# Performance work log

Measured on AMD Instinct MI355X. Metric: run time of the kernel, lower is better.

The kernel has to match this reference:

```python
import jax, jax.numpy as jnp
import numpy as np

N_EXPERTS = 8
D_MODEL = 1024
D_FF = 4096
TOP_K = 2
B, S = 1, 2048


def setup_inputs() -> dict:
    key = jax.random.key(0)
    ks = jax.random.split(key, 5)
    scale_in = 1.0 / np.sqrt(D_MODEL)
    scale_ff = 1.0 / np.sqrt(D_FF)
    return {
        "x": jax.random.normal(ks[0], (B, S, D_MODEL), dtype=jnp.float32),
        "w_gate": jax.random.normal(ks[1], (D_MODEL, N_EXPERTS), dtype=jnp.float32) * scale_in,
        "b_gate": jnp.zeros((N_EXPERTS,), dtype=jnp.float32),
        "w1": jax.random.normal(ks[2], (N_EXPERTS, D_MODEL, D_FF), dtype=jnp.float32) * scale_in,
        "b1": jnp.zeros((N_EXPERTS, D_FF), dtype=jnp.float32),
        "w2": jax.random.normal(ks[3], (N_EXPERTS, D_FF, D_MODEL), dtype=jnp.float32) * scale_ff,
        "b2": jnp.zeros((N_EXPERTS, D_MODEL), dtype=jnp.float32),
    }


def reference(x, w_gate, b_gate, w1, b1, w2, b2):
    d = x.shape[-1]
    xs = x.reshape(-1, d)                       # [T, d]
    T = xs.shape[0]

    # --- routing: top-k gate logits, softmax over the k selected slots ---
    gate_logits = xs @ w_gate + b_gate          # [T, E]
    topk_vals, topk_idx = jax.lax.top_k(gate_logits, TOP_K)   # [T, k]
    weights = jax.nn.softmax(topk_vals, axis=-1)              # [T, k]

    # scatter slot weights into a dense [T, E] combine matrix
    comb = jnp.zeros((T, N_EXPERTS), dtype=xs.dtype)
    comb = comb.at[jnp.arange(T)[:, None], topk_idx].add(weights)

    # --- expert FFNs computed densely, combined with routing weights ---
    h = jax.nn.relu(jnp.einsum('td,edf->etf', xs, w1) + b1[:, None, :])  # [E, T, ff]
    y = jnp.einsum('etf,efd->etd', h, w2) + b2[:, None, :]               # [E, T, d]
    out = jnp.einsum('te,etd->td', comb, y)                              # [T, d]
    return out.reshape(x.shape)
```

## Files before the change

### kernel.cpp

```cpp
#include <hip/hip_runtime.h>
#include <hip/hip_bf16.h>
#include <math.h>

#define T_TOK 2048
#define DM    1024
#define DF    4096
#define NE    8
#define BM    128
#define BN    128
#define BK    64
#define LDA2  72
#define LDAV1 40

typedef __attribute__((ext_vector_type(8))) short          bf16x8;
typedef __attribute__((ext_vector_type(8))) unsigned short ushort8;
typedef __attribute__((ext_vector_type(4))) float          f32x4;

__device__ __forceinline__ unsigned short f2bf(float f) {
  unsigned u = __builtin_bit_cast(unsigned, f);
  unsigned r = u + 0x7fffu + ((u >> 16) & 1u);
  return (unsigned short)(r >> 16);
}

__global__ void convert_x_kernel(const float* __restrict__ x, unsigned short* __restrict__ xb) {
  int i = blockIdx.x * blockDim.x + threadIdx.x;
  const float* src = x + (size_t)i * 8;
  float4 a = *(const float4*)(src);
  float4 b = *(const float4*)(src + 4);
  ushort8 v;
  v[0] = f2bf(a.x); v[1] = f2bf(a.y); v[2] = f2bf(a.z); v[3] = f2bf(a.w);
  v[4] = f2bf(b.x); v[5] = f2bf(b.y); v[6] = f2bf(b.z); v[7] = f2bf(b.w);
  *(ushort8*)(xb + (size_t)i * 8) = v;
}

template<int K, int N>
__global__ __launch_bounds__(256) void transpose_convert_packed(
    const float* __restrict__ W, unsigned short* __restrict__ Wt)
{
  const int e  = blockIdx.z;
  const int kt = blockIdx.y;
  const int nt = blockIdx.x;
  const int k0 = kt * 64;
  const int n0 = nt * 128;
  const float* Wp = W + (size_t)e * K * N;
  __shared__ float Ls[64][129];
  const int tid = threadIdx.x;
  {
    const int kl = tid >> 5;
    const int nl = (tid & 31) * 4;
#pragma unroll
    for (int p = 0; p < 8; p++) {
      const int k = kl + p * 8;
      float4 v = *(const float4*)(Wp + (size_t)(k0 + k) * N + n0 + nl);
      Ls[k][nl + 0] = v.x; Ls[k][nl + 1] = v.y; Ls[k][nl + 2] = v.z; Ls[k][nl + 3] = v.w;
    }
  }
  __syncthreads();
  unsigned short* Wo = Wt + ((((size_t)e * (N / 128) + nt) * (K / 64) + kt) * 128) * 64;
  {
    const int n  = tid & 127;
    const int c0 = tid >> 7;
#pragma unroll
    for (int p = 0; p < 4; p++) {
      const int c = c0 + p * 2;
      ushort8 o;
#pragma unroll
      for (int j = 0; j < 8; j++) o[j] = f2bf(Ls[c * 8 + j][n]);
      *(ushort8*)(Wo + (size_t)n * 64 + c * 8) = o;
    }
  }
}

__global__ __launch_bounds__(256) void gating_kernel(
    const float* __restrict__ x, const float* __restrict__ wg, const float* __restrict__ bg,
    int* __restrict__ cnt, int* __restrict__ perm, float* __restrict__ pw)
{
  int wid  = (blockIdx.x * blockDim.x + threadIdx.x) >> 6;
  int lane = threadIdx.x & 63;
  if (wid >= T_TOK) return;
  const float* xr = x + (size_t)wid * DM;

  float acc[NE];
#pragma unroll
  for (int e = 0; e < NE; e++) acc[e] = 0.f;

  for (int d = lane; d < DM; d += 64) {
    float xv = xr[d];
    const float* wr = wg + (size_t)d * NE;
#pragma unroll
    for (int e = 0; e < NE; e++) acc[e] += xv * wr[e];
  }
#pragma unroll
  for (int off = 32; off > 0; off >>= 1) {
#pragma unroll
    for (int e = 0; e < NE; e++) acc[e] += __shfl_xor(acc[e], off, 64);
  }
  if (lane == 0) {
    float v[NE];
#pragma unroll
    for (int e = 0; e < NE; e++) v[e] = acc[e] + bg[e];
    int i0 = 0; float v0 = v[0];
#pragma unroll
    for (int e = 1; e < NE; e++) { if (v[e] > v0) { v0 = v[e]; i0 = e; } }
    int i1 = -1; float v1 = -INFINITY;
#pragma unroll
    for (int e = 0; e < NE; e++) { if (e != i0 && v[e] > v1) { v1 = v[e]; i1 = e; } }
    float e1 = expf(v1 - v0);
    float s  = 1.f + e1;
    float w0 = 1.f / s, w1 = e1 / s;
    int p0 = atomicAdd(&cnt[i0], 1);
    perm[i0 * T_TOK + p0] = wid; pw[i0 * T_TOK + p0] = w0;
    int p1 = atomicAdd(&cnt[i1], 1);
    perm[i1 * T_TOK + p1] = wid; pw[i1 * T_TOK + p1] = w1;
  }
}

__global__ void pad_scan_kernel(const int* __restrict__ cnt, int* __restrict__ cntpad,
                                int* __restrict__ offs, int* __restrict__ perm, float* __restrict__ pw)
{
  if (threadIdx.x == 0) {
    int o = 0;
    for (int e = 0; e < NE; e++) {
      int c  = cnt[e];
      int cp = (c + BM - 1) / BM * BM;
      cntpad[e] = cp;
      offs[e]   = o;
      o += cp;
    }
    offs[NE] = o;
  }
  for (int e = 0; e < NE; e++) {
    int c  = cnt[e];
    int cp = (c + BM - 1) / BM * BM;
    for (int i = c + threadIdx.x; i < cp; i += blockDim.x) {
      perm[e * T_TOK + i] = 0;
      pw[e * T_TOK + i]   = 0.f;
    }
  }
}

template<int PHASE, int KTOT, int NCOLS, int KSPLIT>
__global__ __launch_bounds__(256, 3) void moe_gemm4(
    const unsigned short* __restrict__ Asrc,
    const unsigned short* __restrict__ Bt,
    const float* __restrict__ bias,
    const int* __restrict__ cntpad, const int* __restrict__ offs,
    const int* __restrict__ perm, const float* __restrict__ pw,
    unsigned short* __restrict__ Hout, float* __restrict__ out)
{
  const int e  = blockIdx.z;
  const int mt = blockIdx.y;
  const int nt = blockIdx.x / KSPLIT;
  const int ks = blockIdx.x % KSPLIT;
  const int cp = cntpad[e];
  if (mt * BM >= cp) return;
  const int tid = threadIdx.x;
  const int oe  = offs[e];

  __shared__ unsigned short As[BM * LDA2];
  __shared__ unsigned short Bs[BN * LDA2];

  const int am = tid >> 1;
  const int ak = (tid & 1) * 32;
  const int kb0 = ks * (KTOT / KSPLIT);
  const int KITERS = (KTOT / KSPLIT) / BK;

  const unsigned short* Ap;
  size_t APITCH;
  if (PHASE == 1) {
    int token = perm[e * T_TOK + mt * BM + am];
    Ap = Asrc + (size_t)token * KTOT + kb0 + ak;
    APITCH = BK;
  } else {
    const size_t rb = (size_t)(oe >> 7) + mt;
    Ap = Asrc + (((rb * (KTOT / 64) + (kb0 >> 6)) * 128 + am) * 64) + ak;
    APITCH = (size_t)128 * 64;
  }
  const unsigned short* Bp =
      Bt + ((((size_t)e * (NCOLS / 128) + nt) * (KTOT / 64) + (kb0 >> 6)) * 128 + am) * 64 + ak;

  const int wid  = tid >> 6;
  const int lane = tid & 63;
  const int wm   = (wid & 1) * 64;
  const int wn   = (wid >> 1) * 64;
  const int lrow = lane & 15;
  const int lk   = (lane >> 4) * 8;

  f32x4 acc[4][4];
#pragma unroll
  for (int i = 0; i < 4; i++)
#pragma unroll
    for (int j = 0; j < 4; j++) acc[i][j] = (f32x4){0.f, 0.f, 0.f, 0.f};

  uint4 pa0, pa1, pa2, pa3, pb0, pb1, pb2, pb3;
  auto LOADT = [&](int kt) {
    const unsigned short* a = Ap + (size_t)kt * APITCH;
    const unsigned short* b = Bp + (size_t)kt * (128 * 64);
    pa0 = *(const uint4*)(a);      pa1 = *(const uint4*)(a + 8);
    pa2 = *(const uint4*)(a + 16); pa3 = *(const uint4*)(a + 24);
    pb0 = *(const uint4*)(b);      pb1 = *(const uint4*)(b + 8);
    pb2 = *(const uint4*)(b + 16); pb3 = *(const uint4*)(b + 24);
  };
  auto STORET = [&]() {
    unsigned short* as = &As[am * LDA2 + ak];
    unsigned short* bs = &Bs[am * LDA2 + ak];
    *(uint4*)(as)      = pa0; *(uint4*)(as + 8)  = pa1;
    *(uint4*)(as + 16) = pa2; *(uint4*)(as + 24) = pa3;
    *(uint4*)(bs)      = pb0; *(uint4*)(bs + 8)  = pb1;
    *(uint4*)(bs + 16) = pb2; *(uint4*)(bs + 24) = pb3;
  };

  LOADT(0);
  STORET();
  for (int kt = 0; kt < KITERS; kt++) {
    __syncthreads();
    if (kt + 1 < KITERS) LOADT(kt + 1);
#pragma unroll
    for (int ksb = 0; ksb < 2; ksb++) {
      bf16x8 af[4], bfr[4];
#pragma unroll
      for (int i = 0; i < 4; i++)
        af[i]  = *(const bf16x8*)&As[(wm + i * 16 + lrow) * LDA2 + ksb * 32 + lk];
#pragma unroll
      for (int j = 0; j < 4; j++)
        bfr[j] = *(const bf16x8*)&Bs[(wn + j * 16 + lrow) * LDA2 + ksb * 32 + lk];
#pragma unroll
      for (int i = 0; i < 4; i++)
#pragma unroll
        for (int j = 0; j < 4; j++)
          acc[i][j] = __builtin_amdgcn_mfma_f32_16x16x32_bf16(af[i], bfr[j], acc[i][j], 0, 0, 0);
    }
    __syncthreads();
    if (kt + 1 < KITERS) STORET();
  }

  const int crow = (lane >> 4) * 4;
  const int ccol = lane & 15;
  const size_t rbh = (size_t)(oe >> 7) + mt;
#pragma unroll
  for (int j = 0; j < 4; j++) {
    const int gn = nt * BN + wn + j * 16 + ccol;
    const float bv = bias[e * NCOLS + gn];
#pragma unroll
    for (int i = 0; i < 4; i++) {
#pragma unroll
      for (int r = 0; r < 4; r++) {
        const int lm = wm + i * 16 + crow + r;
        float v = acc[i][j][r];
        if (PHASE == 1) {
          v += bv;
          v = v > 0.f ? v : 0.f;
          Hout[(((rbh * (NCOLS / 64) + (gn >> 6)) * 128 + lm) * 64) + (gn & 63)] = f2bf(v);
        } else {
          if (ks == 0) v += bv;
          const int li    = e * T_TOK + mt * BM + lm;
          const int token = perm[li];
          const float w   = pw[li];
          atomicAdd(&out[(size_t)token * NCOLS + gn], w * v);
        }
      }
    }
  }
}

template<int PHASE, int KTOT, int NCOLS, int KSPLIT>
__global__ __launch_bounds__(256) void moe_gemm_v1(
    const unsigned short* __restrict__ Asrc,
    const float* __restrict__ Wbase,
    const float* __restrict__ bias,
    const int* __restrict__ cntpad, const int* __restrict__ offs,
    const int* __restrict__ perm, const float* __restrict__ pw,
    unsigned short* __restrict__ Hout, float* __restrict__ out)
{
  const int e  = blockIdx.z;
  const int mt = blockIdx.y;
  const int nt = blockIdx.x / KSPLIT;
  const int ks = blockIdx.x % KSPLIT;
  const int cp = cntpad[e];
  if (mt * BM >= cp) return;
  const int tid = threadIdx.x;
  const int oe  = offs[e];

  __shared__ unsigned short As[BM * LDAV1];
  __shared__ unsigned short Bs[BN * LDAV1];

  const int am = tid >> 1;
  const int ak = (tid & 1) * 16;
  size_t arow_off;
  if (PHASE == 1) {
    int token = perm[e * T_TOK + mt * BM + am];
    arow_off = (size_t)token * KTOT;
  } else {
    arow_off = (size_t)(oe + mt * BM + am) * (size_t)KTOT;
  }
  const int bn  = tid & 127;
  const int bk0 = (tid >> 7) * 16;
  const float* Wexp = Wbase + (size_t)e * KTOT * NCOLS + (size_t)nt * BN;
  const int kbase0 = ks * (KTOT / KSPLIT);
  const int KITERS = (KTOT / KSPLIT) / 32;
  const int wid  = tid >> 6;
  const int lane = tid & 63;
  const int wm   = (wid & 1) * 64;
  const int wn   = (wid >> 1) * 64;
  const int lrow = lane & 15;
  const int lk   = (lane >> 4) * 8;

  f32x4 acc[4][4];
#pragma unroll
  for (int i = 0; i < 4; i++)
#pragma unroll
    for (int j = 0; j < 4; j++) acc[i][j] = (f32x4){0.f, 0.f, 0.f, 0.f};

  for (int kt = 0; kt < KITERS; kt++) {
    const int kb = kbase0 + kt * 32;
    {
      const unsigned short* src = Asrc + arow_off + kb + ak;
      uint4 v0 = *(const uint4*)(src);
      uint4 v1 = *(const uint4*)(src + 8);
      *(uint4*)&As[am * LDAV1 + ak]     = v0;
      *(uint4*)&As[am * LDAV1 + ak + 8] = v1;
    }
#pragma unroll
    for (int t2 = 0; t2 < 2; t2++) {
      const int kk = bk0 + t2 * 8;
      const float* wp = Wexp + (size_t)(kb + kk) * NCOLS + bn;
      ushort8 tv;
#pragma unroll
      for (int j = 0; j < 8; j++) tv[j] = f2bf(wp[(size_t)j * NCOLS]);
      *(ushort8*)&Bs[bn * LDAV1 + kk] = tv;
    }
    __syncthreads();
    bf16x8 af[4], bfr[4];
#pragma unroll
    for (int i = 0; i < 4; i++) af[i]  = *(const bf16x8*)&As[(wm + i * 16 + lrow) * LDAV1 + lk];
#pragma unroll
    for (int j = 0; j < 4; j++) bfr[j] = *(const bf16x8*)&Bs[(wn + j * 16 + lrow) * LDAV1 + lk];
#pragma unroll
    for (int i = 0; i < 4; i++)
#pragma unroll
      for (int j = 0; j < 4; j++)
        acc[i][j] = __builtin_amdgcn_mfma_f32_16x16x32_bf16(af[i], bfr[j], acc[i][j], 0, 0, 0);
    __syncthreads();
  }

  const int crow = (lane >> 4) * 4;
  const int ccol = lane & 15;
#pragma unroll
  for (int j = 0; j < 4; j++) {
    const int gn = nt * BN + wn + j * 16 + ccol;
    const float bv = bias[e * NCOLS + gn];
#pragma unroll
    for (int i = 0; i < 4; i++) {
#pragma unroll
      for (int r = 0; r < 4; r++) {
        const int lm = wm + i * 16 + crow + r;
        float v = acc[i][j][r];
        if (PHASE == 1) {
          v += bv;
          v = v > 0.f ? v : 0.f;
          Hout[(size_t)(oe + mt * BM + lm) * NCOLS + gn] = f2bf(v);
        } else {
          if (ks == 0) v += bv;
          const int li    = e * T_TOK + mt * BM + lm;
          const int token = perm[li];
          const float w   = pw[li];
          atomicAdd(&out[(size_t)token * NCOLS + gn], w * v);
        }
      }
    }
  }
}

extern "C" void kernel_launch(void* const* d_in, const int* in_sizes, int n_in,
                              void* d_out, int out_size, void* d_ws, size_t ws_size,
                              hipStream_t stream) {
  const float* x  = (const float*)d_in[0];
  const float* wg = (const float*)d_in[1];
  const float* bg = (const float*)d_in[2];
  const float* w1 = (const float*)d_in[3];
  const float* b1 = (const float*)d_in[4];
  const float* w2 = (const float*)d_in[5];
  const float* b2 = (const float*)d_in[6];
  float* out = (float*)d_out;

  const size_t XB_BYTES   = (size_t)T_TOK * DM * 2;
  const size_t PERM_BYTES = (size_t)NE * T_TOK * 4;
  const size_t PW_BYTES   = (size_t)NE * T_TOK * 4;
  const size_t H_BYTES    = (size_t)(2 * T_TOK + NE * BM) * DF * 2;
  const size_t W1T_BYTES  = (size_t)NE * DF * DM * 2;
  const size_t W2T_BYTES  = (size_t)NE * DM * DF * 2;

  char* wsp = (char*)d_ws;
  size_t off = 0;
  unsigned short* xb = (unsigned short*)(wsp + off); off += XB_BYTES;
  int*   cnt    = (int*)(wsp + off); off += 256;
  int*   cntpad = cnt + 8;
  int*   offs   = cnt + 16;
  int*   perm   = (int*)(wsp + off);   off += PERM_BYTES;
  float* pwt    = (float*)(wsp + off); off += PW_BYTES;
  unsigned short* H   = (unsigned short*)(wsp + off); off += H_BYTES;
  unsigned short* w1t = (unsigned short*)(wsp + off); off += W1T_BYTES;
  unsigned short* w2t = (unsigned short*)(wsp + off); off += W2T_BYTES;
  const size_t REQUIRED = off;

  hipMemsetAsync(cnt, 0, 256, stream);
  hipMemsetAsync(d_out, 0, (size_t)T_TOK * DM * 4, stream);

  convert_x_kernel<<<(T_TOK * DM / 8) / 256, 256, 0, stream>>>(x, xb);
  gating_kernel<<<T_TOK / 4, 256, 0, stream>>>(x, wg, bg, cnt, perm, pwt);
  pad_scan_kernel<<<1, 256, 0, stream>>>(cnt, cntpad, offs, perm, pwt);

  if (ws_size >= REQUIRED) {
    transpose_convert_packed<DM, DF><<<dim3(DF / 128, DM / 64, NE), 256, 0, stream>>>(w1, w1t);
    transpose_convert_packed<DF, DM><<<dim3(DM / 128, DF / 64, NE), 256, 0, stream>>>(w2, w2t);

    moe_gemm4<1, DM, DF, 1><<<dim3(DF / BN, T_TOK / BM, NE), 256, 0, stream>>>(
        xb, w1t, b1, cntpad, offs, perm, pwt, H, nullptr);
    moe_gemm4<2, DF, DM, 2><<<dim3((DM / BN) * 2, T_TOK / BM, NE), 256, 0, stream>>>(
        H, w2t, b2, cntpad, offs, perm, pwt, nullptr, out);
  } else {
    moe_gemm_v1<1, DM, DF, 1><<<dim3(DF / BN, T_TOK / BM, NE), 256, 0, stream>>>(
        xb, w1, b1, cntpad, offs, perm, pwt, H, nullptr);
    moe_gemm_v1<2, DF, DM, 4><<<dim3((DM / BN) * 4, T_TOK / BM, NE), 256, 0, stream>>>(
        H, w2, b2, cntpad, offs, perm, pwt, nullptr, out);
  }
}
```

Baseline: 629.4 us.

## Replace atomic scatter in second GEMM with split-K buffers and gather combine

The second expert GEMM now writes its per-slot outputs into two dense fp32 buffers, one per K-split, that reuse the w1t workspace, instead of atomically adding weighted results into the output. Gating records each token's slot indices and weights, and a new combine kernel gathers the two expert rows per token, sums the split halves and applies the routing weights. This removes contended fp32 atomics in the GEMM epilogue. In exchange it adds an extra kernel launch and a full write and read of the intermediate buffers. It also relies on w1t being dead after the first GEMM, and the output memset is now redundant.

```diff
diff --git a/kernel.cpp b/kernel.cpp
--- a/kernel.cpp
+++ b/kernel.cpp
@@ -11,6 +11,7 @@
 #define BK    64
 #define LDA2  72
 #define LDAV1 40
+#define YROWS 5120
 
 typedef __attribute__((ext_vector_type(8))) short          bf16x8;
 typedef __attribute__((ext_vector_type(8))) unsigned short ushort8;
@@ -73,7 +74,8 @@
 
 __global__ __launch_bounds__(256) void gating_kernel(
     const float* __restrict__ x, const float* __restrict__ wg, const float* __restrict__ bg,
-    int* __restrict__ cnt, int* __restrict__ perm, float* __restrict__ pw)
+    int* __restrict__ cnt, int* __restrict__ perm, float* __restrict__ pw,
+    int* __restrict__ tok2slot, float* __restrict__ tokw)
 {
   int wid  = (blockIdx.x * blockDim.x + threadIdx.x) >> 6;
   int lane = threadIdx.x & 63;
@@ -112,6 +114,8 @@
     perm[i0 * T_TOK + p0] = wid; pw[i0 * T_TOK + p0] = w0;
     int p1 = atomicAdd(&cnt[i1], 1);
     perm[i1 * T_TOK + p1] = wid; pw[i1 * T_TOK + p1] = w1;
+    tok2slot[2 * wid + 0] = (i0 << 16) | p0;  tokw[2 * wid + 0] = w0;
+    tok2slot[2 * wid + 1] = (i1 << 16) | p1;  tokw[2 * wid + 1] = w1;
   }
 }
 
@@ -139,14 +143,39 @@
   }
 }
 
+__global__ __launch_bounds__(256) void combine_kernel(
+    const float* __restrict__ y0, const float* __restrict__ y1,
+    const int* __restrict__ offs, const int* __restrict__ tok2slot,
+    const float* __restrict__ tokw, float* __restrict__ out)
+{
+  const int t = blockIdx.x;
+  const int d = threadIdx.x * 4;
+  const int s0 = tok2slot[2 * t + 0];
+  const int s1 = tok2slot[2 * t + 1];
+  const float w0 = tokw[2 * t + 0];
+  const float w1 = tokw[2 * t + 1];
+  const size_t r0 = (size_t)(offs[s0 >> 16] + (s0 & 0xffff)) * DM + d;
+  const size_t r1 = (size_t)(offs[s1 >> 16] + (s1 & 0xffff)) * DM + d;
+  float4 a0 = *(const float4*)(y0 + r0);
+  float4 b0 = *(const float4*)(y1 + r0);
+  float4 a1 = *(const float4*)(y0 + r1);
+  float4 b1 = *(const float4*)(y1 + r1);
+  float4 o;
+  o.x = w0 * (a0.x + b0.x) + w1 * (a1.x + b1.x);
+  o.y = w0 * (a0.y + b0.y) + w1 * (a1.y + b1.y);
+  o.z = w0 * (a0.z + b0.z) + w1 * (a1.z + b1.z);
+  o.w = w0 * (a0.w + b0.w) + w1 * (a1.w + b1.w);
+  *(float4*)(out + (size_t)t * DM + d) = o;
+}
+
 template<int PHASE, int KTOT, int NCOLS, int KSPLIT>
-__global__ __launch_bounds__(256, 3) void moe_gemm4(
+__global__ __launch_bounds__(256, 3) void moe_gemm5(
     const unsigned short* __restrict__ Asrc,
     const unsigned short* __restrict__ Bt,
     const float* __restrict__ bias,
     const int* __restrict__ cntpad, const int* __restrict__ offs,
-    const int* __restrict__ perm, const float* __restrict__ pw,
-    unsigned short* __restrict__ Hout, float* __restrict__ out)
+    const int* __restrict__ perm,
+    unsigned short* __restrict__ Hout, float* __restrict__ yout)
 {
   const int e  = blockIdx.z;
   const int mt = blockIdx.y;
@@ -237,6 +266,7 @@
   const int crow = (lane >> 4) * 4;
   const int ccol = lane & 15;
   const size_t rbh = (size_t)(oe >> 7) + mt;
+  float* yp = yout + (size_t)ks * ((size_t)YROWS * NCOLS);
 #pragma unroll
   for (int j = 0; j < 4; j++) {
     const int gn = nt * BN + wn + j * 16 + ccol;
@@ -253,10 +283,7 @@
           Hout[(((rbh * (NCOLS / 64) + (gn >> 6)) * 128 + lm) * 64) + (gn & 63)] = f2bf(v);
         } else {
           if (ks == 0) v += bv;
-          const int li    = e * T_TOK + mt * BM + lm;
-          const int token = perm[li];
-          const float w   = pw[li];
-          atomicAdd(&out[(size_t)token * NCOLS + gn], w * v);
+          yp[(size_t)(oe + mt * BM + lm) * NCOLS + gn] = v;
         }
       }
     }
@@ -386,6 +413,7 @@
   const size_t XB_BYTES   = (size_t)T_TOK * DM * 2;
   const size_t PERM_BYTES = (size_t)NE * T_TOK * 4;
   const size_t PW_BYTES   = (size_t)NE * T_TOK * 4;
+  const size_t TOK_BYTES  = (size_t)T_TOK * 2 * 4;
   const size_t H_BYTES    = (size_t)(2 * T_TOK + NE * BM) * DF * 2;
   const size_t W1T_BYTES  = (size_t)NE * DF * DM * 2;
   const size_t W2T_BYTES  = (size_t)NE * DM * DF * 2;
@@ -398,26 +426,32 @@
   int*   offs   = cnt + 16;
   int*   perm   = (int*)(wsp + off);   off += PERM_BYTES;
   float* pwt    = (float*)(wsp + off); off += PW_BYTES;
+  int*   tok2slot = (int*)(wsp + off);   off += TOK_BYTES;
+  float* tokw     = (float*)(wsp + off); off += TOK_BYTES;
   unsigned short* H   = (unsigned short*)(wsp + off); off += H_BYTES;
   unsigned short* w1t = (unsigned short*)(wsp + off); off += W1T_BYTES;
   unsigned short* w2t = (unsigned short*)(wsp + off); off += W2T_BYTES;
   const size_t REQUIRED = off;
 
+  float* y = (float*)w1t;
+
   hipMemsetAsync(cnt, 0, 256, stream);
   hipMemsetAsync(d_out, 0, (size_t)T_TOK * DM * 4, stream);
 
   convert_x_kernel<<<(T_TOK * DM / 8) / 256, 256, 0, stream>>>(x, xb);
-  gating_kernel<<<T_TOK / 4, 256, 0, stream>>>(x, wg, bg, cnt, perm, pwt);
+  gating_kernel<<<T_TOK / 4, 256, 0, stream>>>(x, wg, bg, cnt, perm, pwt, tok2slot, tokw);
   pad_scan_kernel<<<1, 256, 0, stream>>>(cnt, cntpad, offs, perm, pwt);
 
   if (ws_size >= REQUIRED) {
     transpose_convert_packed<DM, DF><<<dim3(DF / 128, DM / 64, NE), 256, 0, stream>>>(w1, w1t);
     transpose_convert_packed<DF, DM><<<dim3(DM / 128, DF / 64, NE), 256, 0, stream>>>(w2, w2t);
 
-    moe_gemm4<1, DM, DF, 1><<<dim3(DF / BN, T_TOK / BM, NE), 256, 0, stream>>>(
-        xb, w1t, b1, cntpad, offs, perm, pwt, H, nullptr);
-    moe_gemm4<2, DF, DM, 2><<<dim3((DM / BN) * 2, T_TOK / BM, NE), 256, 0, stream>>>(
-        H, w2t, b2, cntpad, offs, perm, pwt, nullptr, out);
+    moe_gemm5<1, DM, DF, 1><<<dim3(DF / BN, T_TOK / BM, NE), 256, 0, stream>>>(
+        xb, w1t, b1, cntpad, offs, perm, H, nullptr);
+    moe_gemm5<2, DF, DM, 2><<<dim3((DM / BN) * 2, T_TOK / BM, NE), 256, 0, stream>>>(
+        H, w2t, b2, cntpad, offs, perm, nullptr, y);
+    combine_kernel<<<T_TOK, 256, 0, stream>>>(
+        y, y + (size_t)YROWS * DM, offs, tok2slot, tokw, out);
   } else {
     moe_gemm_v1<1, DM, DF, 1><<<dim3(DF / BN, T_TOK / BM, NE), 256, 0, stream>>>(
         xb, w1, b1, cntpad, offs, perm, pwt, H, nullptr);
```

Result: faster. 515.8 us (-18.0%).
